# Performance work log

Hardware: AMD Instinct MI355X
Metric: run time of the kernel (lower is better)

The kernel has to match this reference:

```python
import jax, jax.numpy as jnp
import numpy as np

KEY_DIM = 64


def setup_inputs() -> dict:
    key = jax.random.key(0)
    ks = jax.random.split(key, 5)
    B, N, D, H, K, V = 2, 2048, 1024, 16, 64, 64
    scale = 0.02
    return {
        "x": jax.random.normal(ks[0], (B, N, D), dtype=jnp.float32),
        "query_proj": jax.random.normal(ks[1], (H, K, D), dtype=jnp.float32) * scale,
        "key_proj": jax.random.normal(ks[2], (D, K), dtype=jnp.float32) * scale,
        "value_proj": jax.random.normal(ks[3], (D, V), dtype=jnp.float32) * scale,
        "output_proj": jax.random.normal(ks[4], (D, H, V), dtype=jnp.float32) * scale,
    }


def reference(x, query_proj, key_proj, value_proj, output_proj):
    B, D = x.shape[0], x.shape[-1]
    r = x.reshape(B, -1, D)  # [b, n, d] (flatten any spatial dims)
    # MQA: per-head queries, shared single-head K/V
    q = jnp.einsum('bnd,hkd->bnhk', r, query_proj)
    k = jnp.einsum('bmd,dk->bmk', r, key_proj)
    v = jnp.einsum('bmd,dv->bmv', r, value_proj)
    sim = jnp.einsum('bnhk,bmk->bnhm', q, k) / jnp.sqrt(jnp.asarray(KEY_DIM, dtype=r.dtype))
    attn = jax.nn.softmax(sim, axis=-1)  # softmax over key positions m
    o = jnp.einsum('bnhm,bmv->bnhv', attn, v)
    out = jnp.einsum('bnhv,dhv->bnd', o, output_proj)
    return out.reshape(x.shape)
```

## Files before the change

kernel.cpp:

```cpp
#include <hip/hip_runtime.h>
#include <math.h>

typedef __bf16  bf16x8  __attribute__((ext_vector_type(8)));
typedef float   f32x4   __attribute__((ext_vector_type(4)));
typedef ushort  u16x8   __attribute__((ext_vector_type(8)));

static __device__ __forceinline__ ushort f2bf(float f) {
    unsigned u = __float_as_uint(f);
    unsigned r = (u + 0x7fffu + ((u >> 16) & 1u)) >> 16;
    return (ushort)r;
}
static __device__ __forceinline__ unsigned cvt_pk_bf16(float a, float b) {
    unsigned r;
    asm("v_cvt_pk_bf16_f32 %0, %1, %2" : "=v"(r) : "v"(a), "v"(b));
    return r;
}

static __device__ __forceinline__ void gload_lds16(const ushort* g, ushort* l) {
    __builtin_amdgcn_global_load_lds(
        (const __attribute__((address_space(1))) unsigned int*)g,
        (__attribute__((address_space(3))) unsigned int*)l, 16, 0, 0);
}

__global__ __launch_bounds__(256) void convert_kernel(
    const float* __restrict__ x, const float* __restrict__ qp,
    const float* __restrict__ kp, const float* __restrict__ vp,
    const float* __restrict__ op,
    ushort* __restrict__ x_bf, ushort* __restrict__ wall_bf,
    ushort* __restrict__ op_bf)
{
    const int bid = blockIdx.x, t = threadIdx.x;
    if (bid < 4096) {
        const int i = bid * 256 + t;
        const float4 v = ((const float4*)x)[i];
        ushort4 s; s.x = f2bf(v.x); s.y = f2bf(v.y); s.z = f2bf(v.z); s.w = f2bf(v.w);
        ((ushort4*)x_bf)[i] = s;
    } else if (bid < 5120) {
        const int i = (bid - 4096) * 256 + t;
        const float4 v = ((const float4*)qp)[i];
        ushort4 s; s.x = f2bf(v.x); s.y = f2bf(v.y); s.z = f2bf(v.z); s.w = f2bf(v.w);
        ((ushort4*)wall_bf)[i] = s;
    } else if (bid < 6144) {
        const int i = (bid - 5120) * 256 + t;
        const float4 v = ((const float4*)op)[i];
        ushort4 s; s.x = f2bf(v.x); s.y = f2bf(v.y); s.z = f2bf(v.z); s.w = f2bf(v.w);
        ((ushort4*)op_bf)[i] = s;
    } else if (bid < 6400) {
        const int i = (bid - 6144) * 256 + t;
        const int k = i >> 10, d = i & 1023;
        wall_bf[(size_t)(1024 + k) * 1024 + d] = f2bf(kp[(size_t)d * 64 + k]);
    } else {
        const int i = (bid - 6400) * 256 + t;
        const int v = i >> 10, d = i & 1023;
        wall_bf[(size_t)(1088 + v) * 1024 + d] = f2bf(vp[(size_t)d * 64 + v]);
    }
}

template <bool OUT_BF16>
__global__ __launch_bounds__(256) void gemm_mfma_bt(
    const ushort* __restrict__ A, const ushort* __restrict__ Bt,
    void* __restrict__ Cv, int M, int N, int K, int scale_cols, float scale)
{
    __shared__ alignas(16) ushort Asm[2][128 * 32];
    __shared__ alignas(16) ushort Bsm[2][128 * 32];
    const int t  = threadIdx.x;
    const int w  = t >> 6, l = t & 63;
    const int ll = l & 15, lg = l >> 4;
    const int wr = w >> 1, wc = w & 1;

    const int nwg = gridDim.x * gridDim.y;
    int lin = blockIdx.y * gridDim.x + blockIdx.x;
    if ((nwg & 7) == 0) lin = (lin & 7) * (nwg >> 3) + (lin >> 3);
    const int bx = lin % gridDim.x, by = lin / gridDim.x;
    const int m0 = by * 128, n0 = bx * 128;

    f32x4 acc[4][4] = {};

    auto stage = [&](int buf, int k0) {
        #pragma unroll
        for (int i = 0; i < 2; ++i) {
            const int c   = t + i * 256;
            const int row = c >> 2, p = c & 3;
            const int gp  = p ^ ((row >> 1) & 3);
            gload_lds16(&A [(size_t)(m0 + row) * K + k0 + gp * 8], &Asm[buf][c * 8]);
            gload_lds16(&Bt[(size_t)(n0 + row) * K + k0 + gp * 8], &Bsm[buf][c * 8]);
        }
    };

    const int NT = K >> 5;
    stage(0, 0);
    for (int it = 0; it < NT; ++it) {
        const int cur = it & 1;
        if (it + 1 < NT) {
            stage(cur ^ 1, (it + 1) * 32);
            asm volatile("s_waitcnt vmcnt(4)" ::: "memory");
        } else {
            asm volatile("s_waitcnt vmcnt(0)" ::: "memory");
        }
        __builtin_amdgcn_s_barrier();

        bf16x8 af[4], bfr[4];
        #pragma unroll
        for (int mt = 0; mt < 4; ++mt) {
            const int r = wr * 64 + mt * 16 + ll;
            af[mt] = *(const bf16x8*)&Asm[cur][r * 32 + (lg ^ ((r >> 1) & 3)) * 8];
        }
        #pragma unroll
        for (int nt = 0; nt < 4; ++nt) {
            const int r = wc * 64 + nt * 16 + ll;
            bfr[nt] = *(const bf16x8*)&Bsm[cur][r * 32 + (lg ^ ((r >> 1) & 3)) * 8];
        }
        __builtin_amdgcn_s_setprio(1);
        #pragma unroll
        for (int mt = 0; mt < 4; ++mt)
            #pragma unroll
            for (int nt = 0; nt < 4; ++nt)
                acc[mt][nt] = __builtin_amdgcn_mfma_f32_16x16x32_bf16(af[mt], bfr[nt], acc[mt][nt], 0, 0, 0);
        __builtin_amdgcn_s_setprio(0);
        __builtin_amdgcn_s_barrier();
    }

    #pragma unroll
    for (int mt = 0; mt < 4; ++mt) {
        #pragma unroll
        for (int r = 0; r < 4; ++r) {
            const size_t row = m0 + wr * 64 + mt * 16 + lg * 4 + r;
            #pragma unroll
            for (int nt = 0; nt < 4; ++nt) {
                const int col = n0 + wc * 64 + nt * 16 + ll;
                const float f = (col < scale_cols) ? scale : 1.0f;
                const float v = acc[mt][nt][r] * f;
                if (OUT_BF16) ((ushort*)Cv)[row * N + col] = f2bf(v);
                else          ((float *)Cv)[row * N + col] = v;
            }
        }
    }
}

__global__ __launch_bounds__(256) void transpose_v_kernel(
    const ushort* __restrict__ qkv, ushort* __restrict__ vt_bf)
{
    __shared__ alignas(16) ushort tl[64][72];
    const int b  = blockIdx.x >> 5;
    const int m0 = (blockIdx.x & 31) * 64;
    const int t  = threadIdx.x;
    #pragma unroll
    for (int i = 0; i < 2; ++i) {
        const int c = t + i * 256, row = c >> 3, p = c & 7;
        const uint4 v4 = *(const uint4*)&qkv[(size_t)(b * 2048 + m0 + row) * 1152 + 1088 + p * 8];
        const u16x8 v = __builtin_bit_cast(u16x8, v4);
        #pragma unroll
        for (int j = 0; j < 8; ++j) tl[p * 8 + j][row] = v[j];
    }
    __syncthreads();
    #pragma unroll
    for (int i = 0; i < 2; ++i) {
        const int c = t + i * 256, vd = c >> 3, p = c & 7;
        *(uint4*)&vt_bf[(size_t)b * 64 * 2048 + (size_t)vd * 2048 + m0 + p * 8] =
            *(const uint4*)&tl[vd][p * 8];
    }
}

__global__ __launch_bounds__(256) void attn_mfma_kernel(
    const ushort* __restrict__ qkv, const ushort* __restrict__ vt_bf,
    ushort* __restrict__ o_bf)
{
    constexpr int NN = 2048;
    __shared__ alignas(16) ushort Ks[2][64 * 64];
    __shared__ alignas(16) ushort Vs[2][64 * 64];
    __shared__ alignas(16) ushort Ps[4][16 * 64];

    const int qt = blockIdx.x & 31;
    const int h  = (blockIdx.x >> 5) & 15;
    const int b  = blockIdx.x >> 9;
    const int t  = threadIdx.x;
    const int w  = t >> 6, l = t & 63;
    const int lg = l >> 4, ll = l & 15;
    const int q0 = qt * 64 + w * 16;
    const int xr = (ll & 7) << 3;

    bf16x8 qf[2];
    {
        const size_t base = ((size_t)(b * NN) + q0 + ll) * 1152 + h * 64;
        qf[0] = __builtin_bit_cast(bf16x8, *(const uint4*)&qkv[base + lg * 8]);
        qf[1] = __builtin_bit_cast(bf16x8, *(const uint4*)&qkv[base + 32 + lg * 8]);
    }

    f32x4 Ofrag[4] = {};
    float m_run = -1e30f, l_run = 0.f;

    auto stage = [&](int buf, int kv0) {
        #pragma unroll
        for (int i = 0; i < 2; ++i) {
            const int c = t + i * 256;
            const int row = c >> 3, ch = c & 7;
            const int gp = ch ^ (row & 7);
            gload_lds16(&qkv[((size_t)(b * NN) + kv0 + row) * 1152 + 1024 + gp * 8],
                        &Ks[buf][c * 8]);
            gload_lds16(&vt_bf[(size_t)b * 64 * NN + (size_t)row * NN + kv0 + gp * 8],
                        &Vs[buf][c * 8]);
        }
    };

    stage(0, 0);
    asm volatile("s_waitcnt vmcnt(0)" ::: "memory");
    __syncthreads();

    for (int tile = 0; tile < 32; ++tile) {
        const int cur = tile & 1;
        if (tile < 31) stage(cur ^ 1, (tile + 1) * 64);

        const ushort* Kb = &Ks[cur][0];
        const ushort* Vb = &Vs[cur][0];

        f32x4 S[4] = {};
        #pragma unroll
        for (int ks = 0; ks < 2; ++ks) {
            bf16x8 kf[4];
            #pragma unroll
            for (int nt = 0; nt < 4; ++nt)
                kf[nt] = *(const bf16x8*)&Kb[(nt * 16 + ll) * 64 + ((ks * 32 + lg * 8) ^ xr)];
            __builtin_amdgcn_s_setprio(1);
            #pragma unroll
            for (int nt = 0; nt < 4; ++nt)
                S[nt] = __builtin_amdgcn_mfma_f32_16x16x32_bf16(kf[nt], qf[ks], S[nt], 0, 0, 0);
            __builtin_amdgcn_s_setprio(0);
        }

        float pm = S[0][0];
        #pragma unroll
        for (int nt = 0; nt < 4; ++nt)
            #pragma unroll
            for (int r = 0; r < 4; ++r)
                pm = fmaxf(pm, S[nt][r]);
        pm = fmaxf(pm, __shfl_xor(pm, 16));
        pm = fmaxf(pm, __shfl_xor(pm, 32));

        if (__any(pm > m_run + 11.5442f)) {
            const float mnew = fmaxf(m_run, pm);
            const float corr = __builtin_amdgcn_exp2f(m_run - mnew);
            m_run = mnew;
            l_run *= corr;
            #pragma unroll
            for (int r = 0; r < 4; ++r) {
                const float cq = __shfl(corr, lg * 4 + r);
                #pragma unroll
                for (int nt = 0; nt < 4; ++nt) Ofrag[nt][r] *= cq;
            }
        }

        #pragma unroll
        for (int nt = 0; nt < 4; ++nt)
            #pragma unroll
            for (int r = 0; r < 4; ++r) {
                S[nt][r] = __builtin_amdgcn_exp2f(S[nt][r] - m_run);
                l_run += S[nt][r];
            }

        #pragma unroll
        for (int nt = 0; nt < 4; ++nt) {
            uint2 pw;
            pw.x = cvt_pk_bf16(S[nt][0], S[nt][1]);
            pw.y = cvt_pk_bf16(S[nt][2], S[nt][3]);
            *(uint2*)&Ps[w][ll * 64 + ((nt * 16 + lg * 4) ^ xr)] = pw;
        }

        #pragma unroll
        for (int ks = 0; ks < 2; ++ks) {
            const bf16x8 pf = *(const bf16x8*)&Ps[w][ll * 64 + ((ks * 32 + lg * 8) ^ xr)];
            bf16x8 vf[4];
            #pragma unroll
            for (int nt = 0; nt < 4; ++nt)
                vf[nt] = *(const bf16x8*)&Vb[(nt * 16 + ll) * 64 + ((ks * 32 + lg * 8) ^ xr)];
            __builtin_amdgcn_s_setprio(1);
            #pragma unroll
            for (int nt = 0; nt < 4; ++nt)
                Ofrag[nt] = __builtin_amdgcn_mfma_f32_16x16x32_bf16(pf, vf[nt], Ofrag[nt], 0, 0, 0);
            __builtin_amdgcn_s_setprio(0);
        }

        asm volatile("s_waitcnt vmcnt(0)" ::: "memory");
        __syncthreads();
    }

    l_run += __shfl_xor(l_run, 16);
    l_run += __shfl_xor(l_run, 32);
    const float inv = 1.0f / l_run;
    #pragma unroll
    for (int r = 0; r < 4; ++r) {
        const float iq = __shfl(inv, lg * 4 + r);
        const size_t qrow = (size_t)(b * NN) + q0 + lg * 4 + r;
        #pragma unroll
        for (int nt = 0; nt < 4; ++nt)
            o_bf[qrow * 1024 + h * 64 + nt * 16 + ll] = f2bf(Ofrag[nt][r] * iq);
    }
}

extern "C" void kernel_launch(void* const* d_in, const int* in_sizes, int n_in,
                              void* d_out, int out_size, void* d_ws, size_t ws_size,
                              hipStream_t stream)
{
    const float* x  = (const float*)d_in[0];
    const float* qp = (const float*)d_in[1];
    const float* kp = (const float*)d_in[2];
    const float* vp = (const float*)d_in[3];
    const float* op = (const float*)d_in[4];
    float* out = (float*)d_out;

    char* ws = (char*)d_ws;
    ushort* x_bf    = (ushort*)(ws);
    ushort* wall_bf = (ushort*)(ws + 8388608);
    ushort* op_bf   = (ushort*)(ws + 10747904);
    ushort* qkv     = (ushort*)(ws + 12845056);
    ushort* vt_bf   = (ushort*)(ws + 22282240);
    ushort* o_bf    = (ushort*)(ws + 22806528);

    convert_kernel<<<6656, 256, 0, stream>>>(x, qp, kp, vp, op, x_bf, wall_bf, op_bf);
    gemm_mfma_bt<true><<<dim3(1152 / 128, 4096 / 128), 256, 0, stream>>>(
        x_bf, wall_bf, qkv, 4096, 1152, 1024, 1024, 0.18033688f);
    transpose_v_kernel<<<64, 256, 0, stream>>>(qkv, vt_bf);
    attn_mfma_kernel<<<1024, 256, 0, stream>>>(qkv, vt_bf, o_bf);
    gemm_mfma_bt<false><<<dim3(1024 / 128, 4096 / 128), 256, 0, stream>>>(
        o_bf, op_bf, out, 4096, 1024, 1024, 0, 1.0f);
}
```

Baseline: 186.5 us.

## Retile GEMM to 128x64 with BK=64 and transpose PV MFMA output layout

The GEMM kernel moves from 128x128 tiles with K-step 32 to 128x64 tiles with K-step 64. It gets a new 8-chunk XOR swizzle, and the grids double in block count to give more workgroups across CUs. In the attention kernel, the P·V MFMA operands are swapped so each lane owns one query row. This removes the per-row shuffles for the rescale factor and the normalizer, and lets the output be written as packed bf16 pairs. The costs are less reuse per tile for the B operand and more LDS per block.

```diff
diff --git a/kernel.cpp b/kernel.cpp
--- a/kernel.cpp
+++ b/kernel.cpp
@@ -61,8 +61,8 @@
     const ushort* __restrict__ A, const ushort* __restrict__ Bt,
     void* __restrict__ Cv, int M, int N, int K, int scale_cols, float scale)
 {
-    __shared__ alignas(16) ushort Asm[2][128 * 32];
-    __shared__ alignas(16) ushort Bsm[2][128 * 32];
+    __shared__ alignas(16) ushort Asm[2][128 * 64];
+    __shared__ alignas(16) ushort Bsm[2][64 * 64];
     const int t  = threadIdx.x;
     const int w  = t >> 6, l = t & 63;
     const int ll = l & 15, lg = l >> 4;
@@ -72,51 +72,60 @@
     int lin = blockIdx.y * gridDim.x + blockIdx.x;
     if ((nwg & 7) == 0) lin = (lin & 7) * (nwg >> 3) + (lin >> 3);
     const int bx = lin % gridDim.x, by = lin / gridDim.x;
-    const int m0 = by * 128, n0 = bx * 128;
-
-    f32x4 acc[4][4] = {};
+    const int m0 = by * 128, n0 = bx * 64;
+
+    f32x4 acc[4][2] = {};
 
     auto stage = [&](int buf, int k0) {
         #pragma unroll
+        for (int i = 0; i < 4; ++i) {
+            const int c = t + i * 256;
+            const int row = c >> 3, ch = c & 7;
+            const int gp = ch ^ (row & 7);
+            gload_lds16(&A[(size_t)(m0 + row) * K + k0 + gp * 8], &Asm[buf][c * 8]);
+        }
+        #pragma unroll
         for (int i = 0; i < 2; ++i) {
-            const int c   = t + i * 256;
-            const int row = c >> 2, p = c & 3;
-            const int gp  = p ^ ((row >> 1) & 3);
-            gload_lds16(&A [(size_t)(m0 + row) * K + k0 + gp * 8], &Asm[buf][c * 8]);
+            const int c = t + i * 256;
+            const int row = c >> 3, ch = c & 7;
+            const int gp = ch ^ (row & 7);
             gload_lds16(&Bt[(size_t)(n0 + row) * K + k0 + gp * 8], &Bsm[buf][c * 8]);
         }
     };
 
-    const int NT = K >> 5;
+    const int NT = K >> 6;
     stage(0, 0);
     for (int it = 0; it < NT; ++it) {
         const int cur = it & 1;
         if (it + 1 < NT) {
-            stage(cur ^ 1, (it + 1) * 32);
-            asm volatile("s_waitcnt vmcnt(4)" ::: "memory");
+            stage(cur ^ 1, (it + 1) * 64);
+            asm volatile("s_waitcnt vmcnt(6)" ::: "memory");
         } else {
             asm volatile("s_waitcnt vmcnt(0)" ::: "memory");
         }
         __builtin_amdgcn_s_barrier();
 
-        bf16x8 af[4], bfr[4];
-        #pragma unroll
-        for (int mt = 0; mt < 4; ++mt) {
-            const int r = wr * 64 + mt * 16 + ll;
-            af[mt] = *(const bf16x8*)&Asm[cur][r * 32 + (lg ^ ((r >> 1) & 3)) * 8];
-        }
-        #pragma unroll
-        for (int nt = 0; nt < 4; ++nt) {
-            const int r = wc * 64 + nt * 16 + ll;
-            bfr[nt] = *(const bf16x8*)&Bsm[cur][r * 32 + (lg ^ ((r >> 1) & 3)) * 8];
-        }
-        __builtin_amdgcn_s_setprio(1);
-        #pragma unroll
-        for (int mt = 0; mt < 4; ++mt)
-            #pragma unroll
-            for (int nt = 0; nt < 4; ++nt)
-                acc[mt][nt] = __builtin_amdgcn_mfma_f32_16x16x32_bf16(af[mt], bfr[nt], acc[mt][nt], 0, 0, 0);
-        __builtin_amdgcn_s_setprio(0);
+        #pragma unroll
+        for (int ks = 0; ks < 2; ++ks) {
+            bf16x8 af[4], bfr[2];
+            #pragma unroll
+            for (int mt = 0; mt < 4; ++mt) {
+                const int r = wr * 64 + mt * 16 + ll;
+                af[mt] = *(const bf16x8*)&Asm[cur][r * 64 + ((ks * 32 + lg * 8) ^ ((r & 7) * 8))];
+            }
+            #pragma unroll
+            for (int nt = 0; nt < 2; ++nt) {
+                const int r = wc * 32 + nt * 16 + ll;
+                bfr[nt] = *(const bf16x8*)&Bsm[cur][r * 64 + ((ks * 32 + lg * 8) ^ ((r & 7) * 8))];
+            }
+            __builtin_amdgcn_s_setprio(1);
+            #pragma unroll
+            for (int mt = 0; mt < 4; ++mt)
+                #pragma unroll
+                for (int nt = 0; nt < 2; ++nt)
+                    acc[mt][nt] = __builtin_amdgcn_mfma_f32_16x16x32_bf16(af[mt], bfr[nt], acc[mt][nt], 0, 0, 0);
+            __builtin_amdgcn_s_setprio(0);
+        }
         __builtin_amdgcn_s_barrier();
     }
 
@@ -126,8 +135,8 @@
         for (int r = 0; r < 4; ++r) {
             const size_t row = m0 + wr * 64 + mt * 16 + lg * 4 + r;
             #pragma unroll
-            for (int nt = 0; nt < 4; ++nt) {
-                const int col = n0 + wc * 64 + nt * 16 + ll;
+            for (int nt = 0; nt < 2; ++nt) {
+                const int col = n0 + wc * 32 + nt * 16 + ll;
                 const float f = (col < scale_cols) ? scale : 1.0f;
                 const float v = acc[mt][nt][r] * f;
                 if (OUT_BF16) ((ushort*)Cv)[row * N + col] = f2bf(v);
@@ -242,11 +251,9 @@
             m_run = mnew;
             l_run *= corr;
             #pragma unroll
-            for (int r = 0; r < 4; ++r) {
-                const float cq = __shfl(corr, lg * 4 + r);
+            for (int nt = 0; nt < 4; ++nt)
                 #pragma unroll
-                for (int nt = 0; nt < 4; ++nt) Ofrag[nt][r] *= cq;
-            }
+                for (int r = 0; r < 4; ++r) Ofrag[nt][r] *= corr;
         }
 
         #pragma unroll
@@ -275,7 +282,7 @@
             __builtin_amdgcn_s_setprio(1);
             #pragma unroll
             for (int nt = 0; nt < 4; ++nt)
-                Ofrag[nt] = __builtin_amdgcn_mfma_f32_16x16x32_bf16(pf, vf[nt], Ofrag[nt], 0, 0, 0);
+                Ofrag[nt] = __builtin_amdgcn_mfma_f32_16x16x32_bf16(vf[nt], pf, Ofrag[nt], 0, 0, 0);
             __builtin_amdgcn_s_setprio(0);
         }
 
@@ -286,13 +293,15 @@
     l_run += __shfl_xor(l_run, 16);
     l_run += __shfl_xor(l_run, 32);
     const float inv = 1.0f / l_run;
+    const size_t obase = ((size_t)(b * NN) + q0 + ll) * 1024 + h * 64;
     #pragma unroll
-    for (int r = 0; r < 4; ++r) {
-        const float iq = __shfl(inv, lg * 4 + r);
-        const size_t qrow = (size_t)(b * NN) + q0 + lg * 4 + r;
-        #pragma unroll
-        for (int nt = 0; nt < 4; ++nt)
-            o_bf[qrow * 1024 + h * 64 + nt * 16 + ll] = f2bf(Ofrag[nt][r] * iq);
+    for (int nt = 0; nt < 4; ++nt) {
+        #pragma unroll
+        for (int rp = 0; rp < 2; ++rp) {
+            const unsigned pw = cvt_pk_bf16(Ofrag[nt][rp * 2] * inv,
+                                            Ofrag[nt][rp * 2 + 1] * inv);
+            *(unsigned*)&o_bf[obase + nt * 16 + lg * 4 + rp * 2] = pw;
+        }
     }
 }
 
@@ -316,10 +325,10 @@
     ushort* o_bf    = (ushort*)(ws + 22806528);
 
     convert_kernel<<<6656, 256, 0, stream>>>(x, qp, kp, vp, op, x_bf, wall_bf, op_bf);
-    gemm_mfma_bt<true><<<dim3(1152 / 128, 4096 / 128), 256, 0, stream>>>(
+    gemm_mfma_bt<true><<<dim3(1152 / 64, 4096 / 128), 256, 0, stream>>>(
         x_bf, wall_bf, qkv, 4096, 1152, 1024, 1024, 0.18033688f);
     transpose_v_kernel<<<64, 256, 0, stream>>>(qkv, vt_bf);
     attn_mfma_kernel<<<1024, 256, 0, stream>>>(qkv, vt_bf, o_bf);
-    gemm_mfma_bt<false><<<dim3(1024 / 128, 4096 / 128), 256, 0, stream>>>(
+    gemm_mfma_bt<false><<<dim3(1024 / 64, 4096 / 128), 256, 0, stream>>>(
         o_bf, op_bf, out, 4096, 1024, 1024, 0, 1.0f);
 }
```

Result: faster. 174.6 us (-6.3%).
